# Kernel tuning notes

Hardware: AMD Instinct MI355X
Metric: run time of the kernel (lower is better)

The kernel has to match this reference:

```python
import jax, jax.numpy as jnp
import numpy as np

NUM_SPINS = 1024
BATCH = 4096
INPUT_DIM = 2
NUM_HIDDEN = 128
NUM_LAYERS = 1
FIXED_MAG = 0


def setup_inputs() -> dict:
    key = jax.random.key(0)
    ks = jax.random.split(key, 7)
    # spins one-hot encoded, as the module's masking math assumes
    spins = jax.random.randint(ks[0], (NUM_SPINS, BATCH), 0, 2)
    data_in = jax.nn.one_hot(spins, INPUT_DIM, dtype=jnp.float32)
    s = 1.0 / np.sqrt(NUM_HIDDEN)  # torch RNNCell default uniform bound
    W_ih = jax.random.uniform(ks[1], (NUM_HIDDEN, INPUT_DIM), minval=-s, maxval=s, dtype=jnp.float32)
    W_hh = jax.random.uniform(ks[2], (NUM_HIDDEN, NUM_HIDDEN), minval=-s, maxval=s, dtype=jnp.float32)
    b_ih = jax.random.uniform(ks[3], (NUM_HIDDEN,), minval=-s, maxval=s, dtype=jnp.float32)
    b_hh = jax.random.uniform(ks[4], (NUM_HIDDEN,), minval=-s, maxval=s, dtype=jnp.float32)
    W_lin = jax.random.uniform(ks[5], (INPUT_DIM, NUM_HIDDEN), minval=-s, maxval=s, dtype=jnp.float32)
    b_lin = jax.random.uniform(ks[6], (INPUT_DIM,), minval=-s, maxval=s, dtype=jnp.float32)
    return {"data_in": data_in, "W_ih": W_ih, "W_hh": W_hh,
            "b_ih": b_ih, "b_hh": b_hh, "W_lin": W_lin, "b_lin": b_lin}


def reference(data_in, W_ih, W_hh, b_ih, b_hh, W_lin, b_lin):
    S, B, I = data_in.shape
    dt = data_in.dtype
    # input sequence shifted by one spin, first input is init_state [1,0]
    init_state = jnp.array([1.0, 0.0], dtype=dt)
    data = jnp.concatenate([jnp.broadcast_to(init_state, (1, B, I)), data_in[:-1]], axis=0)

    def step(h, x):
        for _ in range(NUM_LAYERS):  # source re-applies the SAME cell num_layers times
            h = jnp.tanh(x @ W_ih.T + b_ih + h @ W_hh.T + b_hh)
        probs = jax.nn.softmax(h @ W_lin.T + b_lin, axis=-1)
        return h, probs

    h0 = jnp.zeros((B, NUM_HIDDEN), dtype=dt)
    _, state_probs = jax.lax.scan(step, h0, data)  # [S, B, I]

    # conditional masking from fixed magnetization
    half = S // 2
    thresh_up = half + (S % 2) + FIXED_MAG // 2
    thresh_down = half - FIXED_MAG // 2
    cum_up = jnp.cumsum(data_in[:, :, 0], axis=0)    # [S, B]
    cum_down = jnp.cumsum(data_in[:, :, 1], axis=0)  # [S, B]
    down_guar = jnp.array([0.0, 1.0], dtype=dt)
    up_guar = jnp.array([1.0, 0.0], dtype=dt)
    mask_up = (cum_up[:-1] >= thresh_up)[..., None]      # for spins 1..S-1
    mask_down = (cum_down[:-1] >= thresh_down)[..., None]
    corr = jnp.where(mask_up, down_guar, state_probs[1:])
    corr = jnp.where(mask_down, up_guar, corr)
    return jnp.concatenate([state_probs[:1], corr], axis=0)
```

## Files before the change

### kernel.cpp

```cpp
#include <hip/hip_runtime.h>

#define NS 1024
#define NB 4096
#define NH 128
#define HLF 512
#define NT 512

typedef __attribute__((ext_vector_type(8))) short short8;
typedef __attribute__((ext_vector_type(4))) float f32x4;

__device__ __forceinline__ short f2bf(float x) {
    unsigned u = __builtin_bit_cast(unsigned, x);
    u = (u + 0x7FFFu + ((u >> 16) & 1u)) >> 16;
    return (short)u;
}
__device__ __forceinline__ float vexp2(float x) {
    float r;
    asm("v_exp_f32 %0, %1" : "=v"(r) : "v"(x));
    return r;
}

#define BARRIER() asm volatile("s_waitcnt lgkmcnt(0)\n\ts_barrier" ::: "memory")
#define MFMA __builtin_amdgcn_mfma_f32_16x16x32_bf16

__global__ __launch_bounds__(NT, 1)
void pwf_kernel(const float* __restrict__ data_in,
                const float* __restrict__ W_ih,
                const float* __restrict__ W_hh,
                const float* __restrict__ b_ih,
                const float* __restrict__ b_hh,
                const float* __restrict__ W_lin,
                const float* __restrict__ b_lin,
                float* __restrict__ out)
{
    __shared__ __align__(16) short hlds[2][16 * NH];
    __shared__ __align__(16) float lp[2][16][4];

    const int tid = threadIdx.x;
    const int w   = tid >> 6;
    const int l   = tid & 63;
    const int g   = l >> 4;
    const int b   = l & 15;
    const int b0  = blockIdx.x * 16;
    const int bb  = b0 + b;
    const int ws  = w & 3;

    const float TL2E = 2.8853900817779268f;
    const float L2E  = 1.4426950408889634f;

    const int hrow = w * 16 + b;
    short8 af0, af1, af2, af3;
    {
        short8 t[4];
        #pragma unroll
        for (int kb = 0; kb < 4; ++kb) {
            const float* src = W_hh + hrow * NH + kb * 32 + g * 8;
            short8 v;
            #pragma unroll
            for (int i = 0; i < 8; ++i) v[i] = f2bf(TL2E * src[i]);
            t[kb] = v;
        }
        af0 = t[0]; af1 = t[1]; af2 = t[2]; af3 = t[3];
    }
    short8 lfrag;
    #pragma unroll
    for (int i = 0; i < 8; ++i) {
        const int k = 32 * ws + 8 * g + i;
        lfrag[i] = (b == 0) ? f2bf(L2E * (W_lin[NH + k] - W_lin[k])) : (short)0;
    }
    float cv0[4], cv1[4];
    #pragma unroll
    for (int r = 0; r < 4; ++r) {
        const int hid = w * 16 + 4 * g + r;
        const float cb = b_ih[hid] + b_hh[hid];
        cv0[r] = TL2E * (W_ih[hid * 2 + 0] + cb);
        cv1[r] = TL2E * (W_ih[hid * 2 + 1] + cb);
    }
    const float blD = L2E * (b_lin[1] - b_lin[0]);

    int aoff[4];
    #pragma unroll
    for (int kb = 0; kb < 4; ++kb)
        aoff[kb] = b * NH + ((kb * 32 + g * 8 + 8 * b) & 127);
    const int aoffP = b * NH + ((32 * ws + 8 * g + 8 * b) & 127);
    const int woffs = b * NH + ((w * 16 + 4 * g + 8 * b) & 127);

    ((uint4*)hlds)[tid] = make_uint4(0u, 0u, 0u, 0u);
    int   cntup = 0, cntdn = 0, sel = 0;
    int   e1u = 0, e1d = 0, e2u = 0, e2d = 0;
    float s0 = data_in[((size_t)0 * NB + bb) * 2];
    float s1 = data_in[((size_t)1 * NB + bb) * 2];
    float s2 = data_in[((size_t)2 * NB + bb) * 2];
    float s3 = data_in[((size_t)3 * NB + bb) * 2];
    BARRIER();

#define STEP(T, P, PH, SU)                                                     \
    {                                                                          \
        const short* hr = hlds[P];                                             \
        short* hw = hlds[(P) ^ 1];                                             \
        const short8 h0 = *(const short8*)&hr[aoff[0]];                        \
        const short8 h1 = *(const short8*)&hr[aoff[1]];                        \
        const short8 h2 = *(const short8*)&hr[aoff[2]];                        \
        const short8 h3 = *(const short8*)&hr[aoff[3]];                        \
        if (w == 4 + (PH)) {                 \
            if ((T) >= 2 && l < 16) {                                          \
                const float4 v = *(const float4*)&lp[(P) ^ 1][l][0];           \
                const float d = v.x + v.y + v.z + v.w + blD;                   \
                float p0 = __builtin_amdgcn_rcpf(1.0f + vexp2(d));             \
                float p1 = 1.0f - p0;                                          \
                if (e2u) { p0 = 0.0f; p1 = 1.0f; }                             \
                if (e2d) { p0 = 1.0f; p1 = 0.0f; }         \
                *(float2*)&out[((size_t)((T) - 2) * NB + b0 + l) * 2] =        \
                    make_float2(p0, p1);                                       \
            }                                                                  \
        }                                                                      \
        if (w < 4) {                      \
            const short8 hp = *(const short8*)&hr[aoffP];                      \
            f32x4 zl = {0.f, 0.f, 0.f, 0.f};                                   \
            const f32x4 cl = MFMA(lfrag, hp, zl, 0, 0, 0);                     \
            if (l < 16) lp[P][l][ws] = cl[0];                                  \
        }                                                                      \
                           \
        f32x4 zz = {0.f, 0.f, 0.f, 0.f};                                       \
        f32x4 c01 = MFMA(af0, h0, zz, 0, 0, 0);                                \
        c01 = MFMA(af1, h1, c01, 0, 0, 0);                                     \
        f32x4 c23 = MFMA(af2, h2, zz, 0, 0, 0);                                \
        c23 = MFMA(af3, h3, c23, 0, 0, 0);                                     \
        e2u = e1u; e2d = e1d;                         \
        e1u = (cntup >= HLF); e1d = (cntdn >= HLF);               \
        float hn[4];                                                           \
        _Pragma("unroll")                                                      \
        for (int r = 0; r < 4; ++r) {                                          \
            const float cv = sel ? cv1[r] : cv0[r];                            \
            const float e  = vexp2(c01[r] + c23[r] + cv);                      \
            hn[r] = fmaf(__builtin_amdgcn_rcpf(e + 1.0f), -2.0f, 1.0f);        \
        }                                                                      \
        unsigned pk01, pk23;                                                   \
        asm("v_cvt_pk_bf16_f32 %0, %1, %2" : "=v"(pk01) : "v"(hn[0]), "v"(hn[1])); \
        asm("v_cvt_pk_bf16_f32 %0, %1, %2" : "=v"(pk23) : "v"(hn[2]), "v"(hn[3])); \
        *(uint2*)&hw[woffs] = make_uint2(pk01, pk23);                          \
        {                               \
            const int isup = ((SU) > 0.5f) ? 1 : 0;                            \
            cntup += isup; cntdn += 1 - isup; sel = 1 - isup;                  \
            const int tn = ((T) + 4 < NS) ? (T) + 4 : NS - 1;                  \
            (SU) = data_in[((size_t)tn * NB + bb) * 2];                        \
        }                                                                      \
        BARRIER();                                                             \
    }

    for (int t = 0; t < NS; t += 4) {
        STEP(t,     0, 0, s0)
        STEP(t + 1, 1, 1, s1)
        STEP(t + 2, 0, 2, s2)
        STEP(t + 3, 1, 3, s3)
    }

    if (w < 4) {
        const short8 hp = *(const short8*)&hlds[0][aoffP];
        f32x4 zl = {0.f, 0.f, 0.f, 0.f};
        const f32x4 cl = MFMA(lfrag, hp, zl, 0, 0, 0);
        if (l < 16) lp[0][l][ws] = cl[0];
    }
    BARRIER();
    if (w == 4 && l < 16) {
        {
            const float4 v = *(const float4*)&lp[1][l][0];
            const float d = v.x + v.y + v.z + v.w + blD;
            float p0 = __builtin_amdgcn_rcpf(1.0f + vexp2(d));
            float p1 = 1.0f - p0;
            if (e2u) { p0 = 0.0f; p1 = 1.0f; }
            if (e2d) { p0 = 1.0f; p1 = 0.0f; }
            *(float2*)&out[((size_t)(NS - 2) * NB + b0 + l) * 2] = make_float2(p0, p1);
        }
        {
            const float4 v = *(const float4*)&lp[0][l][0];
            const float d = v.x + v.y + v.z + v.w + blD;
            float p0 = __builtin_amdgcn_rcpf(1.0f + vexp2(d));
            float p1 = 1.0f - p0;
            if (e1u) { p0 = 0.0f; p1 = 1.0f; }
            if (e1d) { p0 = 1.0f; p1 = 0.0f; }
            *(float2*)&out[((size_t)(NS - 1) * NB + b0 + l) * 2] = make_float2(p0, p1);
        }
    }
}

extern "C" void kernel_launch(void* const* d_in, const int* in_sizes, int n_in,
                              void* d_out, int out_size, void* d_ws, size_t ws_size,
                              hipStream_t stream) {
    const float* data_in = (const float*)d_in[0];
    const float* W_ih    = (const float*)d_in[1];
    const float* W_hh    = (const float*)d_in[2];
    const float* b_ih    = (const float*)d_in[3];
    const float* b_hh    = (const float*)d_in[4];
    const float* W_lin   = (const float*)d_in[5];
    const float* b_lin   = (const float*)d_in[6];
    float* out = (float*)d_out;

    dim3 grid(NB / 16);
    dim3 block(NT);
    pwf_kernel<<<grid, block, 0, stream>>>(data_in, W_ih, W_hh, b_ih, b_hh,
                                           W_lin, b_lin, out);
}
```

Baseline: 436.4 us.

## Split recurrence step into two K-half phases with single LDS hidden buffer

Each timestep is split into two barrier-separated phases over the two K halves of the 128-wide hidden vector. Waves 4-7 finish the tanh for hidden rows 64-127 one phase late, so that work overlaps the next step's first-half MFMAs. The hidden state now lives in a single LDS buffer, and wave 7 computes the output logit directly with four MFMAs, dropping the cross-wave partial-sum reduction through LDS. This doubles the number of barriers per step in exchange for shorter critical-path segments, and it relies on subtle ordering of reads and writes within the single buffer.

```diff
diff --git a/kernel.cpp b/kernel.cpp
--- a/kernel.cpp
+++ b/kernel.cpp
@@ -33,8 +33,7 @@
                 const float* __restrict__ b_lin,
                 float* __restrict__ out)
 {
-    __shared__ __align__(16) short hlds[2][16 * NH];
-    __shared__ __align__(16) float lp[2][16][4];
+    __shared__ __align__(16) short hlds[16 * NH];
 
     const int tid = threadIdx.x;
     const int w   = tid >> 6;
@@ -43,7 +42,6 @@
     const int b   = l & 15;
     const int b0  = blockIdx.x * 16;
     const int bb  = b0 + b;
-    const int ws  = w & 3;
 
     const float TL2E = 2.8853900817779268f;
     const float L2E  = 1.4426950408889634f;
@@ -62,11 +60,20 @@
         }
         af0 = t[0]; af1 = t[1]; af2 = t[2]; af3 = t[3];
     }
-    short8 lfrag;
-    #pragma unroll
-    for (int i = 0; i < 8; ++i) {
-        const int k = 32 * ws + 8 * g + i;
-        lfrag[i] = (b == 0) ? f2bf(L2E * (W_lin[NH + k] - W_lin[k])) : (short)0;
+    short8 lf0, lf1, lf2, lf3;
+    {
+        short8 t[4];
+        #pragma unroll
+        for (int kb = 0; kb < 4; ++kb) {
+            short8 v;
+            #pragma unroll
+            for (int i = 0; i < 8; ++i) {
+                const int k = kb * 32 + g * 8 + i;
+                v[i] = (b == 0) ? f2bf(L2E * (W_lin[NH + k] - W_lin[k])) : (short)0;
+            }
+            t[kb] = v;
+        }
+        lf0 = t[0]; lf1 = t[1]; lf2 = t[2]; lf3 = t[3];
     }
     float cv0[4], cv1[4];
     #pragma unroll
@@ -82,104 +89,145 @@
     #pragma unroll
     for (int kb = 0; kb < 4; ++kb)
         aoff[kb] = b * NH + ((kb * 32 + g * 8 + 8 * b) & 127);
-    const int aoffP = b * NH + ((32 * ws + 8 * g + 8 * b) & 127);
     const int woffs = b * NH + ((w * 16 + 4 * g + 8 * b) & 127);
 
-    ((uint4*)hlds)[tid] = make_uint4(0u, 0u, 0u, 0u);
-    int   cntup = 0, cntdn = 0, sel = 0;
-    int   e1u = 0, e1d = 0, e2u = 0, e2d = 0;
-    float s0 = data_in[((size_t)0 * NB + bb) * 2];
-    float s1 = data_in[((size_t)1 * NB + bb) * 2];
-    float s2 = data_in[((size_t)2 * NB + bb) * 2];
-    float s3 = data_in[((size_t)3 * NB + bb) * 2];
+    ((uint2*)hlds)[tid] = make_uint2(0u, 0u);
+    int   cntup = 0, cntdn = 0, sel = 0, selOld = 0;
+    int   ump = 0, dmp = 0;
+    int   eum = 0, edm = 0;
+    float ediff = 0.0f;
+    f32x4 accA = {0.f, 0.f, 0.f, 0.f}, accB = accA, lg = accA;
+    float sA = data_in[((size_t)0 * NB + bb) * 2];
+    float sB = data_in[((size_t)1 * NB + bb) * 2];
     BARRIER();
 
-#define STEP(T, P, PH, SU)                                                     \
+#define PHASE_A(T)                                                             \
     {                                                                          \
-        const short* hr = hlds[P];                                             \
-        short* hw = hlds[(P) ^ 1];                                             \
-        const short8 h0 = *(const short8*)&hr[aoff[0]];                        \
-        const short8 h1 = *(const short8*)&hr[aoff[1]];                        \
-        const short8 h2 = *(const short8*)&hr[aoff[2]];                        \
-        const short8 h3 = *(const short8*)&hr[aoff[3]];                        \
-        if (w == 4 + (PH)) {                 \
-            if ((T) >= 2 && l < 16) {                                          \
-                const float4 v = *(const float4*)&lp[(P) ^ 1][l][0];           \
-                const float d = v.x + v.y + v.z + v.w + blD;                   \
-                float p0 = __builtin_amdgcn_rcpf(1.0f + vexp2(d));             \
+        const short8 h0 = *(const short8*)&hlds[aoff[0]];                      \
+        const short8 h1 = *(const short8*)&hlds[aoff[1]];                      \
+        if (w >= 4 && (T) >= 1) {        \
+            float hn[4];                                                       \
+            _Pragma("unroll")                                                  \
+            for (int r = 0; r < 4; ++r) {                                      \
+                const float cv = selOld ? cv1[r] : cv0[r];                     \
+                const float e  = vexp2(accA[r] + accB[r] + cv);                \
+                hn[r] = fmaf(__builtin_amdgcn_rcpf(e + 1.0f), -2.0f, 1.0f);    \
+            }                                                                  \
+            unsigned pk01, pk23;                                               \
+            asm("v_cvt_pk_bf16_f32 %0, %1, %2" : "=v"(pk01) : "v"(hn[0]), "v"(hn[1])); \
+            asm("v_cvt_pk_bf16_f32 %0, %1, %2" : "=v"(pk23) : "v"(hn[2]), "v"(hn[3])); \
+            *(uint2*)&hlds[woffs] = make_uint2(pk01, pk23);                    \
+        }                                                                      \
+        if (w == 7) {                                                          \
+            if ((T) >= 2 && l < 16) {             \
+                float p0 = __builtin_amdgcn_rcpf(1.0f + vexp2(ediff));         \
                 float p1 = 1.0f - p0;                                          \
-                if (e2u) { p0 = 0.0f; p1 = 1.0f; }                             \
-                if (e2d) { p0 = 1.0f; p1 = 0.0f; }         \
+                if (eum) { p0 = 0.0f; p1 = 1.0f; }                             \
+                if (edm) { p0 = 1.0f; p1 = 0.0f; }         \
                 *(float2*)&out[((size_t)((T) - 2) * NB + b0 + l) * 2] =        \
                     make_float2(p0, p1);                                       \
             }                                                                  \
-        }                                                                      \
-        if (w < 4) {                      \
-            const short8 hp = *(const short8*)&hr[aoffP];                      \
-            f32x4 zl = {0.f, 0.f, 0.f, 0.f};                                   \
-            const f32x4 cl = MFMA(lfrag, hp, zl, 0, 0, 0);                     \
-            if (l < 16) lp[P][l][ws] = cl[0];                                  \
-        }                                                                      \
-                           \
+            if ((T) >= 1) {                   \
+                f32x4 zl = {0.f, 0.f, 0.f, 0.f};                               \
+                lg = MFMA(lf0, h0, zl, 0, 0, 0);                               \
+                lg = MFMA(lf1, h1, lg, 0, 0, 0);                               \
+            }                                                                  \
+        }                                                                      \
         f32x4 zz = {0.f, 0.f, 0.f, 0.f};                                       \
-        f32x4 c01 = MFMA(af0, h0, zz, 0, 0, 0);                                \
-        c01 = MFMA(af1, h1, c01, 0, 0, 0);                                     \
-        f32x4 c23 = MFMA(af2, h2, zz, 0, 0, 0);                                \
-        c23 = MFMA(af3, h3, c23, 0, 0, 0);                                     \
-        e2u = e1u; e2d = e1d;                         \
-        e1u = (cntup >= HLF); e1d = (cntdn >= HLF);               \
-        float hn[4];                                                           \
-        _Pragma("unroll")                                                      \
-        for (int r = 0; r < 4; ++r) {                                          \
-            const float cv = sel ? cv1[r] : cv0[r];                            \
-            const float e  = vexp2(c01[r] + c23[r] + cv);                      \
-            hn[r] = fmaf(__builtin_amdgcn_rcpf(e + 1.0f), -2.0f, 1.0f);        \
-        }                                                                      \
-        unsigned pk01, pk23;                                                   \
-        asm("v_cvt_pk_bf16_f32 %0, %1, %2" : "=v"(pk01) : "v"(hn[0]), "v"(hn[1])); \
-        asm("v_cvt_pk_bf16_f32 %0, %1, %2" : "=v"(pk23) : "v"(hn[2]), "v"(hn[3])); \
-        *(uint2*)&hw[woffs] = make_uint2(pk01, pk23);                          \
+        accA = MFMA(af0, h0, zz, 0, 0, 0);           \
+        accA = MFMA(af1, h1, accA, 0, 0, 0);                                   \
+        BARRIER();                                                             \
+    }
+
+#define PHASE_B(T, SU)                                                         \
+    {                                                                          \
+        const short8 h2 = *(const short8*)&hlds[aoff[2]];                      \
+        const short8 h3 = *(const short8*)&hlds[aoff[3]];                      \
+        f32x4 zz = {0.f, 0.f, 0.f, 0.f};                                       \
+        accB = MFMA(af2, h2, zz, 0, 0, 0);         \
+        accB = MFMA(af3, h3, accB, 0, 0, 0);                                   \
+        if (w == 7 && (T) >= 1) {        \
+            lg = MFMA(lf2, h2, lg, 0, 0, 0);                                   \
+            lg = MFMA(lf3, h3, lg, 0, 0, 0);                                   \
+            ediff = lg[0] + blD;                                               \
+            eum = ump; edm = dmp;                     \
+        }                                                                      \
+        if (w < 4) {               \
+            float hn[4];                                                       \
+            _Pragma("unroll")                                                  \
+            for (int r = 0; r < 4; ++r) {                                      \
+                const float cv = sel ? cv1[r] : cv0[r];                        \
+                const float e  = vexp2(accA[r] + accB[r] + cv);                \
+                hn[r] = fmaf(__builtin_amdgcn_rcpf(e + 1.0f), -2.0f, 1.0f);    \
+            }                                                                  \
+            unsigned pk01, pk23;                                               \
+            asm("v_cvt_pk_bf16_f32 %0, %1, %2" : "=v"(pk01) : "v"(hn[0]), "v"(hn[1])); \
+            asm("v_cvt_pk_bf16_f32 %0, %1, %2" : "=v"(pk23) : "v"(hn[2]), "v"(hn[3])); \
+            *(uint2*)&hlds[woffs] = make_uint2(pk01, pk23);                    \
+        }                                                                      \
+        ump = (cntup >= HLF);         \
+        dmp = (cntdn >= HLF);                                                  \
+        selOld = sel;                                                          \
         {                               \
             const int isup = ((SU) > 0.5f) ? 1 : 0;                            \
             cntup += isup; cntdn += 1 - isup; sel = 1 - isup;                  \
-            const int tn = ((T) + 4 < NS) ? (T) + 4 : NS - 1;                  \
+            const int tn = ((T) + 2 < NS) ? (T) + 2 : NS - 1;                  \
             (SU) = data_in[((size_t)tn * NB + bb) * 2];                        \
         }                                                                      \
         BARRIER();                                                             \
     }
 
-    for (int t = 0; t < NS; t += 4) {
-        STEP(t,     0, 0, s0)
-        STEP(t + 1, 1, 1, s1)
-        STEP(t + 2, 0, 2, s2)
-        STEP(t + 3, 1, 3, s3)
-    }
-
-    if (w < 4) {
-        const short8 hp = *(const short8*)&hlds[0][aoffP];
-        f32x4 zl = {0.f, 0.f, 0.f, 0.f};
-        const f32x4 cl = MFMA(lfrag, hp, zl, 0, 0, 0);
-        if (l < 16) lp[0][l][ws] = cl[0];
-    }
-    BARRIER();
-    if (w == 4 && l < 16) {
-        {
-            const float4 v = *(const float4*)&lp[1][l][0];
-            const float d = v.x + v.y + v.z + v.w + blD;
-            float p0 = __builtin_amdgcn_rcpf(1.0f + vexp2(d));
+    for (int t = 0; t < NS; t += 2) {
+        PHASE_A(t)
+        PHASE_B(t, sA)
+        PHASE_A(t + 1)
+        PHASE_B(t + 1, sB)
+    }
+
+    {
+        const short8 h0 = *(const short8*)&hlds[aoff[0]];
+        const short8 h1 = *(const short8*)&hlds[aoff[1]];
+        if (w >= 4) {
+            float hn[4];
+            #pragma unroll
+            for (int r = 0; r < 4; ++r) {
+                const float cv = selOld ? cv1[r] : cv0[r];
+                const float e  = vexp2(accA[r] + accB[r] + cv);
+                hn[r] = fmaf(__builtin_amdgcn_rcpf(e + 1.0f), -2.0f, 1.0f);
+            }
+            unsigned pk01, pk23;
+            asm("v_cvt_pk_bf16_f32 %0, %1, %2" : "=v"(pk01) : "v"(hn[0]), "v"(hn[1]));
+            asm("v_cvt_pk_bf16_f32 %0, %1, %2" : "=v"(pk23) : "v"(hn[2]), "v"(hn[3]));
+            *(uint2*)&hlds[woffs] = make_uint2(pk01, pk23);
+        }
+        if (w == 7) {
+            if (l < 16) {
+                float p0 = __builtin_amdgcn_rcpf(1.0f + vexp2(ediff));
+                float p1 = 1.0f - p0;
+                if (eum) { p0 = 0.0f; p1 = 1.0f; }
+                if (edm) { p0 = 1.0f; p1 = 0.0f; }
+                *(float2*)&out[((size_t)(NS - 2) * NB + b0 + l) * 2] =
+                    make_float2(p0, p1);
+            }
+            f32x4 zl = {0.f, 0.f, 0.f, 0.f};
+            lg = MFMA(lf0, h0, zl, 0, 0, 0);
+            lg = MFMA(lf1, h1, lg, 0, 0, 0);
+        }
+        BARRIER();
+    }
+    if (w == 7) {
+        const short8 h2 = *(const short8*)&hlds[aoff[2]];
+        const short8 h3 = *(const short8*)&hlds[aoff[3]];
+        lg = MFMA(lf2, h2, lg, 0, 0, 0);
+        lg = MFMA(lf3, h3, lg, 0, 0, 0);
+        const float fd = lg[0] + blD;
+        if (l < 16) {
+            float p0 = __builtin_amdgcn_rcpf(1.0f + vexp2(fd));
             float p1 = 1.0f - p0;
-            if (e2u) { p0 = 0.0f; p1 = 1.0f; }
-            if (e2d) { p0 = 1.0f; p1 = 0.0f; }
-            *(float2*)&out[((size_t)(NS - 2) * NB + b0 + l) * 2] = make_float2(p0, p1);
-        }
-        {
-            const float4 v = *(const float4*)&lp[0][l][0];
-            const float d = v.x + v.y + v.z + v.w + blD;
-            float p0 = __builtin_amdgcn_rcpf(1.0f + vexp2(d));
-            float p1 = 1.0f - p0;
-            if (e1u) { p0 = 0.0f; p1 = 1.0f; }
-            if (e1d) { p0 = 1.0f; p1 = 0.0f; }
-            *(float2*)&out[((size_t)(NS - 1) * NB + b0 + l) * 2] = make_float2(p0, p1);
+            if (ump) { p0 = 0.0f; p1 = 1.0f; }
+            if (dmp) { p0 = 1.0f; p1 = 0.0f; }
+            *(float2*)&out[((size_t)(NS - 1) * NB + b0 + l) * 2] =
+                make_float2(p0, p1);
         }
     }
 }
```

After: 445.9 us. +2.2%, slower.

## Compute output projection in wave 0 registers, drop LDS partial-sum exchange

Applied to the files above, without the earlier changes.

The output logit-difference projection was split across four waves, with partial sums written to a shared-memory array and reduced by another wave one step later. Wave 0 now does the full four-MFMA projection on the h fragments it already loaded and keeps the result in registers, so the lp array and its cross-wave LDS traffic go away. The bias term is folded into the MFMA accumulator initialisation, the per-step unroll drops from 4 to 2, and data prefetch distance is cut to 2. The cost is that wave 0 carries four extra MFMAs per step, which can lengthen the critical path of the barrier-synchronised recurrence.

```diff
diff --git a/kernel.cpp b/kernel.cpp
--- a/kernel.cpp
+++ b/kernel.cpp
@@ -34,7 +34,6 @@
                 float* __restrict__ out)
 {
     __shared__ __align__(16) short hlds[2][16 * NH];
-    __shared__ __align__(16) float lp[2][16][4];
 
     const int tid = threadIdx.x;
     const int w   = tid >> 6;
@@ -43,7 +42,6 @@
     const int b   = l & 15;
     const int b0  = blockIdx.x * 16;
     const int bb  = b0 + b;
-    const int ws  = w & 3;
 
     const float TL2E = 2.8853900817779268f;
     const float L2E  = 1.4426950408889634f;
@@ -62,11 +60,20 @@
         }
         af0 = t[0]; af1 = t[1]; af2 = t[2]; af3 = t[3];
     }
-    short8 lfrag;
-    #pragma unroll
-    for (int i = 0; i < 8; ++i) {
-        const int k = 32 * ws + 8 * g + i;
-        lfrag[i] = (b == 0) ? f2bf(L2E * (W_lin[NH + k] - W_lin[k])) : (short)0;
+    short8 lf0, lf1, lf2, lf3;
+    {
+        short8 t[4];
+        #pragma unroll
+        for (int kb = 0; kb < 4; ++kb) {
+            short8 v;
+            #pragma unroll
+            for (int i = 0; i < 8; ++i) {
+                const int k = kb * 32 + g * 8 + i;
+                v[i] = (b == 0) ? f2bf(L2E * (W_lin[NH + k] - W_lin[k])) : (short)0;
+            }
+            t[kb] = v;
+        }
+        lf0 = t[0]; lf1 = t[1]; lf2 = t[2]; lf3 = t[3];
     }
     float cv0[4], cv1[4];
     #pragma unroll
@@ -82,104 +89,109 @@
     #pragma unroll
     for (int kb = 0; kb < 4; ++kb)
         aoff[kb] = b * NH + ((kb * 32 + g * 8 + 8 * b) & 127);
-    const int aoffP = b * NH + ((32 * ws + 8 * g + 8 * b) & 127);
     const int woffs = b * NH + ((w * 16 + 4 * g + 8 * b) & 127);
 
     ((uint4*)hlds)[tid] = make_uint4(0u, 0u, 0u, 0u);
     int   cntup = 0, cntdn = 0, sel = 0;
-    int   e1u = 0, e1d = 0, e2u = 0, e2d = 0;
+    int   e1u = 0, e1d = 0;
+    int   eum = 0, edm = 0;
+    float ediff = 0.0f;
     float s0 = data_in[((size_t)0 * NB + bb) * 2];
     float s1 = data_in[((size_t)1 * NB + bb) * 2];
-    float s2 = data_in[((size_t)2 * NB + bb) * 2];
-    float s3 = data_in[((size_t)3 * NB + bb) * 2];
     BARRIER();
 
-#define STEP(T, P, PH, SU)                                                     \
+#define STEP(T, P, SU)                                                         \
     {                                                                          \
         const short* hr = hlds[P];                                             \
         short* hw = hlds[(P) ^ 1];                                             \
+           \
+        f32x4 cini;                                                            \
+        _Pragma("unroll")                                                      \
+        for (int r = 0; r < 4; ++r) cini[r] = sel ? cv1[r] : cv0[r];           \
         const short8 h0 = *(const short8*)&hr[aoff[0]];                        \
         const short8 h1 = *(const short8*)&hr[aoff[1]];                        \
         const short8 h2 = *(const short8*)&hr[aoff[2]];                        \
         const short8 h3 = *(const short8*)&hr[aoff[3]];                        \
-        if (w == 4 + (PH)) {                 \
-            if ((T) >= 2 && l < 16) {                                          \
-                const float4 v = *(const float4*)&lp[(P) ^ 1][l][0];           \
-                const float d = v.x + v.y + v.z + v.w + blD;                   \
-                float p0 = __builtin_amdgcn_rcpf(1.0f + vexp2(d));             \
+        if (w == 0) {                                                          \
+            if ((T) >= 2 && l < 16) {             \
+                float p0 = __builtin_amdgcn_rcpf(1.0f + vexp2(ediff));         \
                 float p1 = 1.0f - p0;                                          \
-                if (e2u) { p0 = 0.0f; p1 = 1.0f; }                             \
-                if (e2d) { p0 = 1.0f; p1 = 0.0f; }         \
+                if (eum) { p0 = 0.0f; p1 = 1.0f; }                             \
+                if (edm) { p0 = 1.0f; p1 = 0.0f; }         \
                 *(float2*)&out[((size_t)((T) - 2) * NB + b0 + l) * 2] =        \
                     make_float2(p0, p1);                                       \
             }                                                                  \
+            if ((T) >= 1) {        \
+                f32x4 li = {blD, blD, blD, blD};                               \
+                f32x4 zl = {0.f, 0.f, 0.f, 0.f};                               \
+                f32x4 cl01 = MFMA(lf0, h0, li, 0, 0, 0);                       \
+                cl01 = MFMA(lf1, h1, cl01, 0, 0, 0);                           \
+                f32x4 cl23 = MFMA(lf2, h2, zl, 0, 0, 0);                       \
+                cl23 = MFMA(lf3, h3, cl23, 0, 0, 0);                           \
+                ediff = cl01[0] + cl23[0];            \
+                eum = e1u; edm = e1d;                 \
+            }                                                                  \
         }                                                                      \
-        if (w < 4) {                      \
-            const short8 hp = *(const short8*)&hr[aoffP];                      \
-            f32x4 zl = {0.f, 0.f, 0.f, 0.f};                                   \
-            const f32x4 cl = MFMA(lfrag, hp, zl, 0, 0, 0);                     \
-            if (l < 16) lp[P][l][ws] = cl[0];                                  \
-        }                                                                      \
-                           \
+        e1u = (cntup >= HLF);             \
+        e1d = (cntdn >= HLF);                                                  \
+            \
         f32x4 zz = {0.f, 0.f, 0.f, 0.f};                                       \
-        f32x4 c01 = MFMA(af0, h0, zz, 0, 0, 0);                                \
+        f32x4 c01 = MFMA(af0, h0, cini, 0, 0, 0);                              \
         c01 = MFMA(af1, h1, c01, 0, 0, 0);                                     \
         f32x4 c23 = MFMA(af2, h2, zz, 0, 0, 0);                                \
         c23 = MFMA(af3, h3, c23, 0, 0, 0);                                     \
-        e2u = e1u; e2d = e1d;                         \
-        e1u = (cntup >= HLF); e1d = (cntdn >= HLF);               \
         float hn[4];                                                           \
         _Pragma("unroll")                                                      \
         for (int r = 0; r < 4; ++r) {                                          \
-            const float cv = sel ? cv1[r] : cv0[r];                            \
-            const float e  = vexp2(c01[r] + c23[r] + cv);                      \
+            const float e = vexp2(c01[r] + c23[r]);                            \
             hn[r] = fmaf(__builtin_amdgcn_rcpf(e + 1.0f), -2.0f, 1.0f);        \
         }                                                                      \
         unsigned pk01, pk23;                                                   \
         asm("v_cvt_pk_bf16_f32 %0, %1, %2" : "=v"(pk01) : "v"(hn[0]), "v"(hn[1])); \
         asm("v_cvt_pk_bf16_f32 %0, %1, %2" : "=v"(pk23) : "v"(hn[2]), "v"(hn[3])); \
-        *(uint2*)&hw[woffs] = make_uint2(pk01, pk23);                          \
-        {                               \
+        *(uint2*)&hw[woffs] = make_uint2(pk01, pk23);    \
+        {          \
             const int isup = ((SU) > 0.5f) ? 1 : 0;                            \
             cntup += isup; cntdn += 1 - isup; sel = 1 - isup;                  \
-            const int tn = ((T) + 4 < NS) ? (T) + 4 : NS - 1;                  \
+            const int tn = ((T) + 2 < NS) ? (T) + 2 : NS - 1;                  \
             (SU) = data_in[((size_t)tn * NB + bb) * 2];                        \
         }                                                                      \
         BARRIER();                                                             \
     }
 
-    for (int t = 0; t < NS; t += 4) {
-        STEP(t,     0, 0, s0)
-        STEP(t + 1, 1, 1, s1)
-        STEP(t + 2, 0, 2, s2)
-        STEP(t + 3, 1, 3, s3)
-    }
-
-    if (w < 4) {
-        const short8 hp = *(const short8*)&hlds[0][aoffP];
+    for (int t = 0; t < NS; t += 2) {
+        STEP(t, 0, s0)
+        STEP(t + 1, 1, s1)
+    }
+
+    if (w == 0) {
+        if (l < 16) {
+            float p0 = __builtin_amdgcn_rcpf(1.0f + vexp2(ediff));
+            float p1 = 1.0f - p0;
+            if (eum) { p0 = 0.0f; p1 = 1.0f; }
+            if (edm) { p0 = 1.0f; p1 = 0.0f; }
+            *(float2*)&out[((size_t)(NS - 2) * NB + b0 + l) * 2] =
+                make_float2(p0, p1);
+        }
+        const short* hr = hlds[0];
+        const short8 h0 = *(const short8*)&hr[aoff[0]];
+        const short8 h1 = *(const short8*)&hr[aoff[1]];
+        const short8 h2 = *(const short8*)&hr[aoff[2]];
+        const short8 h3 = *(const short8*)&hr[aoff[3]];
+        f32x4 li = {blD, blD, blD, blD};
         f32x4 zl = {0.f, 0.f, 0.f, 0.f};
-        const f32x4 cl = MFMA(lfrag, hp, zl, 0, 0, 0);
-        if (l < 16) lp[0][l][ws] = cl[0];
-    }
-    BARRIER();
-    if (w == 4 && l < 16) {
-        {
-            const float4 v = *(const float4*)&lp[1][l][0];
-            const float d = v.x + v.y + v.z + v.w + blD;
-            float p0 = __builtin_amdgcn_rcpf(1.0f + vexp2(d));
-            float p1 = 1.0f - p0;
-            if (e2u) { p0 = 0.0f; p1 = 1.0f; }
-            if (e2d) { p0 = 1.0f; p1 = 0.0f; }
-            *(float2*)&out[((size_t)(NS - 2) * NB + b0 + l) * 2] = make_float2(p0, p1);
-        }
-        {
-            const float4 v = *(const float4*)&lp[0][l][0];
-            const float d = v.x + v.y + v.z + v.w + blD;
-            float p0 = __builtin_amdgcn_rcpf(1.0f + vexp2(d));
+        f32x4 cl01 = MFMA(lf0, h0, li, 0, 0, 0);
+        cl01 = MFMA(lf1, h1, cl01, 0, 0, 0);
+        f32x4 cl23 = MFMA(lf2, h2, zl, 0, 0, 0);
+        cl23 = MFMA(lf3, h3, cl23, 0, 0, 0);
+        const float fd = cl01[0] + cl23[0];
+        if (l < 16) {
+            float p0 = __builtin_amdgcn_rcpf(1.0f + vexp2(fd));
             float p1 = 1.0f - p0;
             if (e1u) { p0 = 0.0f; p1 = 1.0f; }
             if (e1d) { p0 = 1.0f; p1 = 0.0f; }
-            *(float2*)&out[((size_t)(NS - 1) * NB + b0 + l) * 2] = make_float2(p0, p1);
+            *(float2*)&out[((size_t)(NS - 1) * NB + b0 + l) * 2] =
+                make_float2(p0, p1);
         }
     }
 }
```

New measurement: 381.6 us (median of 2 runs). 12.6% less time.
